# Optimization experiments

Hardware: AMD Instinct MI355X
Metric: run time of the kernel (lower is better)

The kernel has to match this reference:

```python
import jax, jax.numpy as jnp
import numpy as np

NEG = -9.0e9  # the -9000000000.0 sentinel used by the torch code


def _masked_bidir_scores(first, second, fmask, smask):
    """Vectorized form of the BxB python double loop in score_grounding.
    first: (B,N,D), second: (B,L,D), fmask: (B,N), smask: (B,L).
    Returns sent_scores (B,B) and mention_scores (B,N,L) (= diagonal att)."""
    mask = fmask[:, None, :, None] * smask[None, :, None, :]          # (B,B,N,L)
    avg = jnp.where(mask != 0, mask, NEG)
    am_first = jax.nn.softmax(avg, axis=2)                            # softmax over N (dim=0 per pair)
    am_second = jax.nn.softmax(avg, axis=3)                           # softmax over L (dim=1 per pair)
    dot = jnp.einsum('ind,jld->ijnl', first, second)                  # (B,B,N,L)
    attm = dot * mask
    att = jnp.where(attm * mask != 0, attm, NEG)
    aw_first = jax.nn.softmax(att, axis=3) * mask                     # softmax(att, dim=-1)*mask
    aw_second = jnp.transpose(
        jax.nn.softmax(jnp.swapaxes(att, 2, 3), axis=3) * jnp.swapaxes(mask, 2, 3), (0, 1, 3, 2)
    )                                                                 # softmax(att.T,-1)*mask.T, transposed back
    sent = (jnp.sum(aw_first * att * am_first, axis=(2, 3))
            + jnp.sum(aw_second * att * am_second, axis=(2, 3)))      # (B,B)
    B = first.shape[0]
    mention = att[jnp.arange(B), jnp.arange(B)]                       # diagonal pairs (B,N,L)
    return sent, mention


def _pairwise_mlp(first, second, W1, b1, W2, b2, W3, b3):
    # SimplePairWiseClassifier: MLP over cat(first, second, first*second); dropout=0 (eval-deterministic)
    x = jnp.concatenate([first, second, first * second], axis=-1)     # (..., 3D)
    h = jax.nn.relu(x @ W1 + b1)
    h = jax.nn.relu(h @ W2 + b2)
    return (h @ W3 + b3)[..., 0]


def setup_inputs() -> dict:
    key = jax.random.key(0)
    ks = jax.random.split(key, 12)
    B, Nt, Ns, L, D, H = 32, 64, 48, 36, 1024, 1024

    def mask(k, n):
        m = (jax.random.uniform(k, (B, n)) < 0.85).astype(jnp.float32)
        return m.at[:, :2].set(1.0)  # guarantee no all-zero rows

    return {
        'text_embeddings': jax.random.normal(ks[0], (B, Nt, D), jnp.float32),
        'span_embeddings': jax.random.normal(ks[1], (B, Ns, D), jnp.float32),
        'image_embeddings': jax.random.normal(ks[2], (B, L, D), jnp.float32),
        'text_mask': mask(ks[3], Nt),
        'span_mask': mask(ks[4], Ns),
        'image_mask': mask(ks[5], L),
        'W1': jax.random.normal(ks[6], (3 * D, H), jnp.float32) * 0.02,
        'b1': jnp.zeros((H,), jnp.float32),
        'W2': jax.random.normal(ks[7], (H, H), jnp.float32) * 0.02,
        'b2': jnp.zeros((H,), jnp.float32),
        'W3': jax.random.normal(ks[8], (H, 1), jnp.float32) * 0.02,
        'b3': jnp.zeros((1,), jnp.float32),
    }


def reference(text_embeddings, span_embeddings, image_embeddings,
              text_mask, span_mask, image_mask, W1, b1, W2, b2, W3, b3):
    B, Ns, D = span_embeddings.shape
    # calculate_loss
    S, _ = _masked_bidir_scores(text_embeddings, image_embeddings, text_mask, image_mask)
    # span_emb.view(B, N, -1, D).mean(dim=2) is identity for (B,Ns,D)
    _, grounding_scores = _masked_bidir_scores(span_embeddings, image_embeddings, span_mask, image_mask)
    # score_text over all span pairs (itertools.combinations order == triu_indices k=1)
    fi, si = np.triu_indices(Ns, k=1)
    text_scores = _pairwise_mlp(span_embeddings[:, fi], span_embeddings[:, si],
                                W1, b1, W2, b2, W3, b3)               # (B, Ns*(Ns-1)/2)
    # contrastive retrieval loss over the BxB sentence-image score matrix
    loss = -(jnp.trace(jax.nn.log_softmax(S, axis=1))
             + jnp.trace(jax.nn.log_softmax(S.T, axis=1))) / B
    return loss, grounding_scores, text_scores
```

## Files before the change

kernel.cpp:

```cpp
#include <hip/hip_runtime.h>
#include <math.h>
#include <stdint.h>

#define B_    32
#define NT    64
#define NS    48
#define LI    36
#define D_    1024
#define H_    1024
#define NPAIR 1128
#define ROWS  (B_*NPAIR)
#define NEGV  -9.0e9f
#define NROWT 282
#define CPX   36

typedef _Float16 half8 __attribute__((ext_vector_type(8)));
typedef float floatx4 __attribute__((ext_vector_type(4)));
typedef __attribute__((address_space(3))) uint32_t lds_u32;
typedef __attribute__((address_space(1))) const uint32_t glb_u32;

#define GLOAD16(src, dst) __builtin_amdgcn_global_load_lds((glb_u32*)(src), (lds_u32*)(dst), 16, 0, 0)

#define MMQ(QR, QC)                                                            \
  {                                                                            \
    _Pragma("unroll") for (int i = 0; i < 4; ++i) {                            \
      _Pragma("unroll") for (int j = 0; j < 2; ++j) {                          \
        acc[QR * 4 + i][QC * 2 + j] = __builtin_amdgcn_mfma_f32_16x16x32_f16(  \
            aF[i][0], bF[j][0], acc[QR * 4 + i][QC * 2 + j], 0, 0, 0);         \
        acc[QR * 4 + i][QC * 2 + j] = __builtin_amdgcn_mfma_f32_16x16x32_f16(  \
            aF[i][1], bF[j][1], acc[QR * 4 + i][QC * 2 + j], 0, 0, 0);         \
      }                                                                        \
    }                                                                          \
  }

__global__ __launch_bounds__(512, 2) void gemm2_8ph(
    const _Float16* __restrict__ Am, const _Float16* __restrict__ Bt,
    float* __restrict__ scores, const float* __restrict__ bias,
    const float* __restrict__ W3) {
  __shared__ __align__(16) _Float16 sP[65536];
  __shared__ float sRed[256][4];

  const int orig = blockIdx.x;
  const int xcd = orig & 7, pos = orig >> 3;
  const int wg = (xcd < 4 ? xcd * 71 : 284 + (xcd - 4) * 70) + pos;
  const int rowBase = (wg >> 2) * 256;
  const int colBase = (wg & 3) * 256;

  const int t = threadIdx.x;
  const int wave = t >> 6, lane = t & 63;
  const int wq_r = wave >> 2, wq_c = wave & 3;
  const int l15 = lane & 15, l16 = lane >> 4;
  const int sxor = l15 & 7;

  const int srow0 = t >> 3, srow1 = (512 + t) >> 3;
  const int lcol0 = ((t & 7) ^ (srow0 & 7)) << 3;
  const int lcol1 = (((512 + t) & 7) ^ (srow1 & 7)) << 3;
  const _Float16* aS0 = Am + (size_t)(rowBase + srow0) * D_ + lcol0;
  const _Float16* aS1 = Am + (size_t)(rowBase + srow1) * D_ + lcol1;
  const _Float16* bS0 = Bt + (size_t)(colBase + srow0) * D_ + lcol0;
  const _Float16* bS1 = Bt + (size_t)(colBase + srow1) * D_ + lcol1;

  auto stgA = [&](int kt, int h) {
    const int db = kt & 1;
    const size_t so = (size_t)kt * 64 + (size_t)h * 128 * D_;
    _Float16* d = sP + ((db << 1) + h) * 8192;
    GLOAD16(aS0 + so, d + t * 8);
    GLOAD16(aS1 + so, d + 4096 + t * 8);
  };
  auto stgB = [&](int kt, int h) {
    const int db = kt & 1;
    const size_t so = (size_t)kt * 64 + (size_t)h * 128 * D_;
    _Float16* d = sP + 32768 + ((db << 1) + h) * 8192;
    GLOAD16(bS0 + so, d + t * 8);
    GLOAD16(bS1 + so, d + 4096 + t * 8);
  };

  const int aRdRow = (wq_r * 64 + l15) * 64;
  const int bRdRow = (wq_c * 32 + l15) * 64;
  const int rdSlot0 = ((l16) ^ sxor) << 3;
  const int rdSlot1 = ((4 + l16) ^ sxor) << 3;

  half8 aF[4][2], bF[2][2];
  floatx4 acc[8][4] = {};

  auto ldA = [&](int db, int qr) {
    const _Float16* p = sP + ((db << 1) + qr) * 8192 + aRdRow;
#pragma unroll
    for (int i = 0; i < 4; ++i) {
      aF[i][0] = *(const half8*)(p + i * 1024 + rdSlot0);
      aF[i][1] = *(const half8*)(p + i * 1024 + rdSlot1);
    }
  };
  auto ldB = [&](int db, int qc) {
    const _Float16* p = sP + 32768 + ((db << 1) + qc) * 8192 + bRdRow;
#pragma unroll
    for (int j = 0; j < 2; ++j) {
      bF[j][0] = *(const half8*)(p + j * 1024 + rdSlot0);
      bF[j][1] = *(const half8*)(p + j * 1024 + rdSlot1);
    }
  };

  stgB(0, 0); stgA(0, 1); stgA(0, 0); stgB(0, 1); stgB(1, 0); stgA(1, 1);
  asm volatile("s_waitcnt vmcnt(4)" ::: "memory");
  __builtin_amdgcn_s_barrier();

#pragma unroll 1
  for (int kt = 0; kt < 16; ++kt) {
    const int db = kt & 1;
    const int kn1 = (kt + 1) & 15, kn2 = (kt + 2) & 15;
    ldA(db, 0); ldB(db, 0);
    stgA(kn1, 0);
    __builtin_amdgcn_sched_barrier(0);
    __builtin_amdgcn_s_barrier();
    __builtin_amdgcn_s_setprio(1);
    MMQ(0, 0);
    __builtin_amdgcn_s_setprio(0);
    __builtin_amdgcn_s_barrier();
    ldA(db, 1);
    stgB(kn1, 1);
    __builtin_amdgcn_sched_barrier(0);
    __builtin_amdgcn_s_barrier();
    __builtin_amdgcn_s_setprio(1);
    MMQ(1, 0);
    __builtin_amdgcn_s_setprio(0);
    __builtin_amdgcn_s_barrier();
    ldB(db, 1);
    stgB(kn2, 0);
    __builtin_amdgcn_sched_barrier(0);
    __builtin_amdgcn_s_barrier();
    __builtin_amdgcn_s_setprio(1);
    MMQ(1, 1);
    __builtin_amdgcn_s_setprio(0);
    __builtin_amdgcn_s_barrier();
    ldA(db, 0);
    stgA(kn2, 1);
    __builtin_amdgcn_sched_barrier(0);
    asm volatile("s_waitcnt vmcnt(4)" ::: "memory");
    __builtin_amdgcn_s_barrier();
    __builtin_amdgcn_s_setprio(1);
    MMQ(0, 1);
    __builtin_amdgcn_s_setprio(0);
    __builtin_amdgcn_s_barrier();
  }

  float bv[2][2], wv[2][2];
#pragma unroll
  for (int qc = 0; qc < 2; ++qc)
#pragma unroll
    for (int j = 0; j < 2; ++j) {
      int c = colBase + qc * 128 + wq_c * 32 + j * 16 + l15;
      bv[qc][j] = bias[c];
      wv[qc][j] = W3[c];
    }
#pragma unroll
  for (int qr = 0; qr < 2; ++qr)
#pragma unroll
    for (int i = 0; i < 4; ++i)
#pragma unroll
      for (int q = 0; q < 4; ++q) {
        float s = 0.f;
#pragma unroll
        for (int qc = 0; qc < 2; ++qc)
#pragma unroll
          for (int j = 0; j < 2; ++j)
            s += fmaxf(acc[qr * 4 + i][qc * 2 + j][q] + bv[qc][j], 0.f) * wv[qc][j];
        s += __shfl_xor(s, 1); s += __shfl_xor(s, 2);
        s += __shfl_xor(s, 4); s += __shfl_xor(s, 8);
        if (l15 == 0)
          sRed[qr * 128 + wq_r * 64 + i * 16 + l16 * 4 + q][wq_c] = s;
      }
  __syncthreads();
  if (t < 256)
    atomicAdd(&scores[rowBase + t],
              sRed[t][0] + sRed[t][1] + sRed[t][2] + sRed[t][3]);
}

__device__ __forceinline__ void gemm_body(
    const _Float16* __restrict__ A, const _Float16* __restrict__ Bt,
    float* __restrict__ Cf, int N, int K, int rowBase, int colBase) {
  __shared__ __align__(16) _Float16 sA[8192];
  __shared__ __align__(16) _Float16 sB[8192];
  const int tid = threadIdx.x;
  const int lane = tid & 63;
  const int wave = tid >> 6;
  const int wr = wave >> 1, wc = wave & 1;
  const int l15 = lane & 15, l16 = lane >> 4;
  const int rsw = (l15 >> 1) & 3;
  const int sRow = tid >> 2;
  const int swz8 = (((tid & 3) ^ ((tid >> 3) & 3)) << 3);
  const _Float16* gA = A + (size_t)(rowBase + sRow) * K + swz8;
  const _Float16* gB = Bt + (size_t)(colBase + sRow) * K + swz8;
  _Float16* lA = sA + tid * 8;
  _Float16* lB = sB + tid * 8;

  floatx4 acc[4][4] = {};
  for (int k0 = 0; k0 < K; k0 += 64) {
    GLOAD16(gA + k0,               lA);
    GLOAD16(gA + 64 * K + k0,      lA + 2048);
    GLOAD16(gA + k0 + 32,          lA + 4096);
    GLOAD16(gA + 64 * K + k0 + 32, lA + 6144);
    GLOAD16(gB + k0,               lB);
    GLOAD16(gB + 64 * K + k0,      lB + 2048);
    GLOAD16(gB + k0 + 32,          lB + 4096);
    GLOAD16(gB + 64 * K + k0 + 32, lB + 6144);
    __syncthreads();
#pragma unroll
    for (int h = 0; h < 2; ++h) {
      const int hb = h * 4096;
      half8 aF[4], bF[4];
#pragma unroll
      for (int i = 0; i < 4; ++i)
        aF[i] = *(const half8*)&sA[hb + (wr * 64 + i * 16 + l15) * 32 + ((l16 ^ rsw) << 3)];
#pragma unroll
      for (int j = 0; j < 4; ++j)
        bF[j] = *(const half8*)&sB[hb + (wc * 64 + j * 16 + l15) * 32 + ((l16 ^ rsw) << 3)];
#pragma unroll
      for (int i = 0; i < 4; ++i)
#pragma unroll
        for (int j = 0; j < 4; ++j)
          acc[i][j] = __builtin_amdgcn_mfma_f32_16x16x32_f16(aF[i], bF[j], acc[i][j], 0, 0, 0);
    }
    __syncthreads();
  }
#pragma unroll
  for (int i = 0; i < 4; ++i)
#pragma unroll
    for (int q = 0; q < 4; ++q) {
      int r = rowBase + wr * 64 + i * 16 + l16 * 4 + q;
#pragma unroll
      for (int j = 0; j < 4; ++j) {
        int c = colBase + wc * 64 + j * 16 + l15;
        Cf[(size_t)r * N + c] = acc[i][j][q];
      }
    }
}

__global__ __launch_bounds__(256) void gemm_trio(
    const _Float16* __restrict__ textH, const _Float16* __restrict__ imgH,
    const _Float16* __restrict__ spanH, const _Float16* __restrict__ W1abT,
    float* __restrict__ dotTI, float* __restrict__ dotSI, float* __restrict__ AB1) {
  int bid = blockIdx.x;
  if (bid < 144)      gemm_body(textH, imgH, dotTI, 1152, D_, (bid / 9) * 128, (bid % 9) * 128);
  else if (bid < 252) { int b = bid - 144; gemm_body(spanH, imgH, dotSI, 1152, D_, (b / 9) * 128, (b % 9) * 128); }
  else                { int b = bid - 252; gemm_body(spanH, W1abT, AB1, 2048, D_, (b / 16) * 128, (b % 16) * 128); }
}

__global__ __launch_bounds__(256) void gemm1_fused(
    const _Float16* __restrict__ spanH, const _Float16* __restrict__ W1cT,
    const float* __restrict__ AB1, const float* __restrict__ b1,
    _Float16* __restrict__ h1out,
    const int* __restrict__ idxF, const int* __restrict__ idxS) {
  __shared__ __align__(16) _Float16 sF[8192];
  __shared__ __align__(16) _Float16 sS[8192];
  __shared__ __align__(16) _Float16 sB[8192];
  __shared__ int sIF[128], sIS[128];
  int bid = blockIdx.x;
  int x = bid & 7, ord = bid >> 3;
  int rowT = x * CPX + (ord >> 3);
  int colT = ord & 7;
  if (rowT >= NROWT) return;
  const int rowBase = rowT * 128, colBase = colT * 128;
  const int tid = threadIdx.x;
  const int lane = tid & 63;
  const int wave = tid >> 6;
  const int wr = wave >> 1, wc = wave & 1;
  const int l15 = lane & 15, l16 = lane >> 4;
  const int rsw = (l15 >> 1) & 3;

  if (tid < 128) {
    int rg = rowBase + tid;
    sIF[tid] = idxF[rg];
    sIS[tid] = idxS[rg];
  }
  __syncthreads();

  const int sRow = tid >> 2;
  const int swz8 = (((tid & 3) ^ ((tid >> 3) & 3)) << 3);
  const _Float16* gF0 = spanH + (size_t)sIF[sRow] * D_ + swz8;
  const _Float16* gF1 = spanH + (size_t)sIF[sRow + 64] * D_ + swz8;
  const _Float16* gS0 = spanH + (size_t)sIS[sRow] * D_ + swz8;
  const _Float16* gS1 = spanH + (size_t)sIS[sRow + 64] * D_ + swz8;
  const _Float16* gB  = W1cT + (size_t)(colBase + sRow) * D_ + swz8;
  _Float16* lF = sF + tid * 8;
  _Float16* lS = sS + tid * 8;
  _Float16* lB = sB + tid * 8;

  floatx4 acc[4][4] = {};
  for (int k0 = 0; k0 < D_; k0 += 64) {
    GLOAD16(gF0 + k0,      lF);
    GLOAD16(gF1 + k0,      lF + 2048);
    GLOAD16(gF0 + k0 + 32, lF + 4096);
    GLOAD16(gF1 + k0 + 32, lF + 6144);
    GLOAD16(gS0 + k0,      lS);
    GLOAD16(gS1 + k0,      lS + 2048);
    GLOAD16(gS0 + k0 + 32, lS + 4096);
    GLOAD16(gS1 + k0 + 32, lS + 6144);
    GLOAD16(gB + k0,               lB);
    GLOAD16(gB + 64 * D_ + k0,     lB + 2048);
    GLOAD16(gB + k0 + 32,          lB + 4096);
    GLOAD16(gB + 64 * D_ + k0 + 32,lB + 6144);
    __syncthreads();
#pragma unroll
    for (int h = 0; h < 2; ++h) {
      const int hb = h * 4096;
      half8 aF[4], bF[4];
#pragma unroll
      for (int i = 0; i < 4; ++i) {
        int off = hb + (wr * 64 + i * 16 + l15) * 32 + ((l16 ^ rsw) << 3);
        half8 f = *(const half8*)&sF[off];
        half8 s = *(const half8*)&sS[off];
        aF[i] = f * s;
      }
#pragma unroll
      for (int j = 0; j < 4; ++j)
        bF[j] = *(const half8*)&sB[hb + (wc * 64 + j * 16 + l15) * 32 + ((l16 ^ rsw) << 3)];
#pragma unroll
      for (int i = 0; i < 4; ++i)
#pragma unroll
        for (int j = 0; j < 4; ++j)
          acc[i][j] = __builtin_amdgcn_mfma_f32_16x16x32_f16(aF[i], bF[j], acc[i][j], 0, 0, 0);
    }
    __syncthreads();
  }

  int cols[4]; float bv[4];
#pragma unroll
  for (int j = 0; j < 4; ++j) {
    cols[j] = colBase + wc * 64 + j * 16 + l15;
    bv[j] = b1[cols[j]];
  }
#pragma unroll
  for (int i = 0; i < 4; ++i)
#pragma unroll
    for (int q = 0; q < 4; ++q) {
      int rL = wr * 64 + i * 16 + l16 * 4 + q;
      int rG = rowBase + rL;
      const float* ap = AB1 + (size_t)sIF[rL] * 2048;
      const float* bp = AB1 + (size_t)sIS[rL] * 2048 + 1024;
#pragma unroll
      for (int j = 0; j < 4; ++j) {
        int c = cols[j];
        float v = acc[i][j][q] + ap[c] + bp[c] + bv[j];
        h1out[(size_t)rG * 1024 + c] = (_Float16)fmaxf(v, 0.f);
      }
    }
}

__global__ __launch_bounds__(256) void cvt_all(
    const float* __restrict__ text, const float* __restrict__ span,
    const float* __restrict__ img, _Float16* __restrict__ textH,
    _Float16* __restrict__ spanH, _Float16* __restrict__ imgH) {
  long long i = (long long)blockIdx.x * 256 + threadIdx.x;
  const float* src; _Float16* dst; long long off;
  if (i < 262144)      { src = text; dst = textH; off = i; }
  else if (i < 458752) { src = span; dst = spanH; off = i - 262144; }
  else if (i < 606208) { src = img;  dst = imgH;  off = i - 458752; }
  else return;
  const float4* p = (const float4*)src + off * 2;
  float4 a = p[0], b = p[1];
  half8 h;
  h[0] = (_Float16)a.x; h[1] = (_Float16)a.y; h[2] = (_Float16)a.z; h[3] = (_Float16)a.w;
  h[4] = (_Float16)b.x; h[5] = (_Float16)b.y; h[6] = (_Float16)b.z; h[7] = (_Float16)b.w;
  *(half8*)(dst + off * 8) = h;
}

__global__ __launch_bounds__(256) void transpose_all(
    const float* __restrict__ W1, const float* __restrict__ W2,
    _Float16* __restrict__ W1abT, _Float16* __restrict__ W1cT,
    _Float16* __restrict__ W2T) {
  __shared__ float tbuf[32][33];
  const float* in; _Float16* out;
  switch (blockIdx.z) {
    case 0: in = W1;                 out = W1abT;                 break;
    case 1: in = W1 + 1024 * 1024;   out = W1abT + 1024 * 1024;   break;
    case 2: in = W1 + 2048 * 1024;   out = W1cT;                  break;
    default: in = W2;                out = W2T;                   break;
  }
  const int tx = threadIdx.x & 31, ty = threadIdx.x >> 5;
  const int k0 = blockIdx.y * 32, n0 = blockIdx.x * 32;
#pragma unroll
  for (int q = 0; q < 4; ++q)
    tbuf[ty + q * 8][tx] = in[(size_t)(k0 + ty + q * 8) * 1024 + n0 + tx];
  __syncthreads();
#pragma unroll
  for (int q = 0; q < 4; ++q)
    out[(size_t)(n0 + ty + q * 8) * 1024 + k0 + tx] = (_Float16)tbuf[tx][ty + q * 8];
}

__global__ __launch_bounds__(256) void idx_init(int* __restrict__ idxF, int* __restrict__ idxS) {
  int r = blockIdx.x * 256 + threadIdx.x;
  if (r >= ROWS) return;
  int bb = r / NPAIR, p = r - bb * NPAIR;
  int cum = 0, f = 0;
  while (true) { int cnt = NS - 1 - f; if (p < cum + cnt) break; cum += cnt; ++f; }
  idxF[r] = bb * NS + f;
  idxS[r] = bb * NS + f + 1 + (p - cum);
}

__global__ void init_scores(float* __restrict__ scores, const float* __restrict__ b3) {
  int idx = blockIdx.x * 256 + threadIdx.x;
  if (idx < ROWS) scores[idx] = b3[0];
}

__global__ __launch_bounds__(256) void extract_grounding(
    const float* __restrict__ dotSI, const float* __restrict__ smask,
    const float* __restrict__ imask, float* __restrict__ outg) {
  int idx = blockIdx.x * 256 + threadIdx.x;
  if (idx >= B_ * NS * LI) return;
  int b = idx / (NS * LI);
  int rem = idx - b * (NS * LI);
  int n = rem / LI, l = rem - n * LI;
  float v = dotSI[(size_t)(b * NS + n) * (B_ * LI) + b * LI + l];
  outg[idx] = (smask[b * NS + n] * imask[b * LI + l] != 0.f) ? v : NEGV;
}

__global__ __launch_bounds__(64) void sent_kernel(
    const float* __restrict__ dotTI, const float* __restrict__ tmask,
    const float* __restrict__ imask, float* __restrict__ S) {
  const int i = blockIdx.y, j = blockIdx.x, t = threadIdx.x;
  __shared__ float red1[64], red2[64];
  const int stride = B_ * LI;
  float e1 = 0.f;
  {
    float tm = tmask[i * NT + t];
    if (tm != 0.f) {
      const float* row = dotTI + (size_t)(i * NT + t) * stride + j * LI;
      float m = -INFINITY;
      for (int l = 0; l < LI; ++l) if (imask[j * LI + l] != 0.f) m = fmaxf(m, row[l]);
      float z = 0.f, w = 0.f;
      for (int l = 0; l < LI; ++l) if (imask[j * LI + l] != 0.f) {
        float d = row[l], p = expf(d - m);
        z += p; w += p * d;
      }
      e1 = w / z;
    }
  }
  red1[t] = e1;
  float e2 = 0.f;
  if (t < LI) {
    float im = imask[j * LI + t];
    if (im != 0.f) {
      const float* col = dotTI + (size_t)(i * NT) * stride + j * LI + t;
      float m = -INFINITY;
      for (int n = 0; n < NT; ++n) if (tmask[i * NT + n] != 0.f) m = fmaxf(m, col[(size_t)n * stride]);
      float z = 0.f, w = 0.f;
      for (int n = 0; n < NT; ++n) if (tmask[i * NT + n] != 0.f) {
        float d = col[(size_t)n * stride], p = expf(d - m);
        z += p; w += p * d;
      }
      e2 = w / z;
    }
  }
  red2[t] = e2;
  __syncthreads();
  if (t == 0) {
    float s1 = 0.f, s2 = 0.f, cn = 0.f, cl = 0.f;
    for (int n = 0; n < NT; ++n) { s1 += red1[n]; cn += tmask[i * NT + n]; }
    for (int l = 0; l < LI; ++l) { s2 += red2[l]; cl += imask[j * LI + l]; }
    S[i * B_ + j] = s1 / cn + s2 / cl;
  }
}

__global__ __launch_bounds__(64) void loss_kernel(
    const float* __restrict__ S, float* __restrict__ out) {
  __shared__ float sS[B_][B_ + 1];
  __shared__ float acc[B_];
  const int t = threadIdx.x;
  for (int e = t; e < B_ * B_; e += 64) sS[e / B_][e % B_] = S[e];
  __syncthreads();
  if (t < B_) {
    float m = -INFINITY;
    for (int j = 0; j < B_; ++j) m = fmaxf(m, sS[t][j]);
    float z = 0.f;
    for (int j = 0; j < B_; ++j) z += expf(sS[t][j] - m);
    float lr = m + logf(z);
    float m2 = -INFINITY;
    for (int i = 0; i < B_; ++i) m2 = fmaxf(m2, sS[i][t]);
    float z2 = 0.f;
    for (int i = 0; i < B_; ++i) z2 += expf(sS[i][t] - m2);
    float lc = m2 + logf(z2);
    acc[t] = 2.f * sS[t][t] - lr - lc;
  }
  __syncthreads();
  if (t == 0) {
    float s = 0.f;
    for (int i = 0; i < B_; ++i) s += acc[i];
    out[0] = -s / (float)B_;
  }
}

extern "C" void kernel_launch(void* const* d_in, const int* in_sizes, int n_in,
                              void* d_out, int out_size, void* d_ws, size_t ws_size,
                              hipStream_t stream) {
  const float* text  = (const float*)d_in[0];
  const float* span  = (const float*)d_in[1];
  const float* img   = (const float*)d_in[2];
  const float* tmask = (const float*)d_in[3];
  const float* smask = (const float*)d_in[4];
  const float* imask = (const float*)d_in[5];
  const float* W1    = (const float*)d_in[6];
  const float* b1    = (const float*)d_in[7];
  const float* W2    = (const float*)d_in[8];
  const float* b2    = (const float*)d_in[9];
  const float* W3    = (const float*)d_in[10];
  const float* b3    = (const float*)d_in[11];

  float* out     = (float*)d_out;
  float* outLoss = out;
  float* outG    = out + 1;
  float* outT    = out + 1 + (size_t)B_ * NS * LI;

  char* w = (char*)d_ws;
  float*    dotTI = (float*)w;            w += (size_t)(B_*NT) * (B_*LI) * 4;
  float*    dotSI = (float*)w;            w += (size_t)(B_*NS) * (B_*LI) * 4;
  float*    S     = (float*)w;            w += 1024 * 4;
  float*    AB1   = (float*)w;            w += (size_t)1536 * 2048 * 4;
  _Float16* h1    = (_Float16*)w;         w += (size_t)ROWS * 1024 * 2;
  _Float16* textH = (_Float16*)w;         w += (size_t)2048 * 1024 * 2;
  _Float16* spanH = (_Float16*)w;         w += (size_t)1536 * 1024 * 2;
  _Float16* imgH  = (_Float16*)w;         w += (size_t)1152 * 1024 * 2;
  _Float16* W1abT = (_Float16*)w;         w += (size_t)2048 * 1024 * 2;
  _Float16* W1cT  = (_Float16*)w;         w += (size_t)1024 * 1024 * 2;
  _Float16* W2T   = (_Float16*)w;         w += (size_t)1024 * 1024 * 2;
  int*      idxF  = (int*)w;              w += ROWS * 4;
  int*      idxS  = (int*)w;              w += ROWS * 4;
  (void)ws_size; (void)in_sizes; (void)n_in; (void)out_size;

  cvt_all<<<(606208 + 255) / 256, 256, 0, stream>>>(text, span, img, textH, spanH, imgH);
  transpose_all<<<dim3(32, 32, 4), 256, 0, stream>>>(W1, W2, W1abT, W1cT, W2T);
  idx_init<<<(ROWS + 255) / 256, 256, 0, stream>>>(idxF, idxS);

  gemm_trio<<<444, 256, 0, stream>>>(textH, imgH, spanH, W1abT, dotTI, dotSI, AB1);
  sent_kernel<<<dim3(B_, B_), 64, 0, stream>>>(dotTI, tmask, imask, S);
  loss_kernel<<<1, 64, 0, stream>>>(S, outLoss);
  extract_grounding<<<(B_*NS*LI + 255) / 256, 256, 0, stream>>>(dotSI, smask, imask, outG);

  gemm1_fused<<<8 * CPX * 8, 256, 0, stream>>>(spanH, W1cT, AB1, b1, h1, idxF, idxS);
  init_scores<<<(ROWS + 255) / 256, 256, 0, stream>>>(outT, b3);
  gemm2_8ph<<<564, 512, 0, stream>>>(h1, W2T, outT, b2, W3);
}
```

Baseline: 331.1 us.

## Replace gather GEMM1 with 256x256 8-phase pipelined kernel using register-staged products

The old 128x128 gemm1_fused kernel is replaced by gemm1_8ph, a 512-thread 256x256-tile kernel. It uses the same phased MFMA schedule with setprio and XCD-aware block remapping as gemm2. Gathered span rows are loaded into registers, multiplied elementwise, and written once to LDS as the A operand, while the weight tiles go through direct global-to-LDS loads. This removes the per-MFMA re-multiplication of F and S from LDS and halves the operand traffic per output, at the cost of more registers and tighter manual waitcnt sequencing. gemm2's prefetch index masking is also moved inside the staging helpers.

```diff
diff --git a/kernel.cpp b/kernel.cpp
--- a/kernel.cpp
+++ b/kernel.cpp
@@ -11,8 +11,6 @@
 #define NPAIR 1128
 #define ROWS  (B_*NPAIR)
 #define NEGV  -9.0e9f
-#define NROWT 282
-#define CPX   36
 
 typedef _Float16 half8 __attribute__((ext_vector_type(8)));
 typedef float floatx4 __attribute__((ext_vector_type(4)));
@@ -33,6 +31,167 @@
     }                                                                          \
   }
 
+__global__ __launch_bounds__(512, 2) void gemm1_8ph(
+    const _Float16* __restrict__ spanH, const _Float16* __restrict__ W1cT,
+    const float* __restrict__ AB1, const float* __restrict__ b1,
+    _Float16* __restrict__ h1out,
+    const int* __restrict__ idxF, const int* __restrict__ idxS) {
+  __shared__ __align__(16) _Float16 sP[32768];
+  __shared__ int sIF[256], sIS[256];
+
+  const int orig = blockIdx.x;
+  const int xcd = orig & 7, pos = orig >> 3;
+  const int wg = (xcd < 4 ? xcd * 71 : 284 + (xcd - 4) * 70) + pos;
+  const int rowBase = (wg >> 2) * 256;
+  const int colBase = (wg & 3) * 256;
+
+  const int t = threadIdx.x;
+  const int wave = t >> 6, lane = t & 63;
+  const int wq_r = wave >> 2, wq_c = wave & 3;
+  const int l15 = lane & 15, l16 = lane >> 4;
+
+  if (t < 256) { sIF[t] = idxF[rowBase + t]; sIS[t] = idxS[rowBase + t]; }
+  __syncthreads();
+
+  const int srow = t >> 3;
+  const int slot = t & 7;
+  const int wsw = ((slot ^ (srow & 7)) << 3);
+
+  const int oF0a = sIF[srow] << 10,        oF0b = sIF[64 + srow] << 10;
+  const int oS0a = sIS[srow] << 10,        oS0b = sIS[64 + srow] << 10;
+  const int oF1a = sIF[128 + srow] << 10,  oF1b = sIF[192 + srow] << 10;
+  const int oS1a = sIS[128 + srow] << 10,  oS1b = sIS[192 + srow] << 10;
+  const int lcol = slot << 3;
+
+  const _Float16* gB0a = W1cT + (size_t)(colBase + srow) * D_ + wsw;
+  const _Float16* gB0b = W1cT + (size_t)(colBase + 64 + srow) * D_ + wsw;
+  const _Float16* gB1a = W1cT + (size_t)(colBase + 128 + srow) * D_ + wsw;
+  const _Float16* gB1b = W1cT + (size_t)(colBase + 192 + srow) * D_ + wsw;
+
+  half8 rF0a, rF0b, rS0a, rS0b, rF1a, rF1b, rS1a, rS1b;
+
+  #define ISSUE_FS0(kt) {                                            \
+    const int kc = (((kt) & 15) << 6) + lcol;                        \
+    rF0a = *(const half8*)(spanH + oF0a + kc);                       \
+    rF0b = *(const half8*)(spanH + oF0b + kc);                       \
+    rS0a = *(const half8*)(spanH + oS0a + kc);                       \
+    rS0b = *(const half8*)(spanH + oS0b + kc); }
+  #define ISSUE_FS1(kt) {                                            \
+    const int kc = (((kt) & 15) << 6) + lcol;                        \
+    rF1a = *(const half8*)(spanH + oF1a + kc);                       \
+    rF1b = *(const half8*)(spanH + oF1b + kc);                       \
+    rS1a = *(const half8*)(spanH + oS1a + kc);                       \
+    rS1b = *(const half8*)(spanH + oS1b + kc); }
+  #define WRITE_A0() {                                               \
+    *(half8*)(sP + srow * 64 + wsw)        = rF0a * rS0a;            \
+    *(half8*)(sP + 4096 + srow * 64 + wsw) = rF0b * rS0b; }
+  #define WRITE_A1() {                                               \
+    *(half8*)(sP + 8192 + srow * 64 + wsw)  = rF1a * rS1a;           \
+    *(half8*)(sP + 12288 + srow * 64 + wsw) = rF1b * rS1b; }
+  #define STG_B0(kt) {                                               \
+    const int kc = (((kt) & 15) << 6);                               \
+    GLOAD16(gB0a + kc, sP + 16384 + t * 8);                          \
+    GLOAD16(gB0b + kc, sP + 20480 + t * 8); }
+  #define STG_B1(kt) {                                               \
+    const int kc = (((kt) & 15) << 6);                               \
+    GLOAD16(gB1a + kc, sP + 24576 + t * 8);                          \
+    GLOAD16(gB1b + kc, sP + 28672 + t * 8); }
+
+  const int rsw = l15 & 7;
+  const int aRd = (wq_r * 64 + l15) * 64;
+  const int bRd = (wq_c * 32 + l15) * 64;
+  const int rd0 = ((l16) ^ rsw) << 3;
+  const int rd1 = ((4 + l16) ^ rsw) << 3;
+  half8 aF[4][2], bF[2][2];
+  floatx4 acc[8][4] = {};
+  #define LDA(h) {                                                   \
+    const _Float16* p = sP + (h) * 8192 + aRd;                       \
+    _Pragma("unroll") for (int i = 0; i < 4; ++i) {                  \
+      aF[i][0] = *(const half8*)(p + i * 1024 + rd0);                \
+      aF[i][1] = *(const half8*)(p + i * 1024 + rd1); } }
+  #define LDB(h) {                                                   \
+    const _Float16* p = sP + 16384 + (h) * 8192 + bRd;               \
+    _Pragma("unroll") for (int j = 0; j < 2; ++j) {                  \
+      bF[j][0] = *(const half8*)(p + j * 1024 + rd0);                \
+      bF[j][1] = *(const half8*)(p + j * 1024 + rd1); } }
+
+  ISSUE_FS0(0); ISSUE_FS1(0); STG_B0(0);
+  asm volatile("s_waitcnt vmcnt(6)" ::: "memory");
+  WRITE_A0();
+  asm volatile("s_waitcnt lgkmcnt(0)" ::: "memory");
+  __builtin_amdgcn_sched_barrier(0);
+  __builtin_amdgcn_s_barrier();
+
+#pragma unroll 1
+  for (int kt = 0; kt < 16; ++kt) {
+    STG_B1(kt);
+    ISSUE_FS0(kt + 1);
+    asm volatile("s_waitcnt vmcnt(6)" ::: "memory");
+    WRITE_A1();
+    LDA(0); LDB(0);
+    asm volatile("s_waitcnt lgkmcnt(0)" ::: "memory");
+    __builtin_amdgcn_sched_barrier(0);
+    __builtin_amdgcn_s_barrier();
+    __builtin_amdgcn_s_setprio(1);
+    MMQ(0, 0);
+    __builtin_amdgcn_s_setprio(0);
+    __builtin_amdgcn_s_barrier();
+    ISSUE_FS1(kt + 1);
+    LDA(1);
+    __builtin_amdgcn_sched_barrier(0);
+    __builtin_amdgcn_s_barrier();
+    __builtin_amdgcn_s_setprio(1);
+    MMQ(1, 0);
+    __builtin_amdgcn_s_setprio(0);
+    __builtin_amdgcn_s_barrier();
+    STG_B0(kt + 1);
+    asm volatile("s_waitcnt vmcnt(10)" ::: "memory");
+    LDA(0); LDB(1);
+    __builtin_amdgcn_sched_barrier(0);
+    __builtin_amdgcn_s_barrier();
+    __builtin_amdgcn_s_setprio(1);
+    MMQ(0, 1);
+    __builtin_amdgcn_s_setprio(0);
+    __builtin_amdgcn_s_barrier();
+    asm volatile("s_waitcnt vmcnt(6)" ::: "memory");
+    WRITE_A0();
+    LDA(1);
+    asm volatile("s_waitcnt lgkmcnt(0)" ::: "memory");
+    __builtin_amdgcn_sched_barrier(0);
+    __builtin_amdgcn_s_barrier();
+    __builtin_amdgcn_s_setprio(1);
+    MMQ(1, 1);
+    __builtin_amdgcn_s_setprio(0);
+    __builtin_amdgcn_s_barrier();
+  }
+
+  float bv[2][2];
+#pragma unroll
+  for (int qc = 0; qc < 2; ++qc)
+#pragma unroll
+    for (int j = 0; j < 2; ++j)
+      bv[qc][j] = b1[colBase + qc * 128 + wq_c * 32 + j * 16 + l15];
+#pragma unroll
+  for (int qr = 0; qr < 2; ++qr)
+#pragma unroll
+    for (int i = 0; i < 4; ++i)
+#pragma unroll
+      for (int q = 0; q < 4; ++q) {
+        int rL = qr * 128 + wq_r * 64 + i * 16 + l16 * 4 + q;
+        const float* ap = AB1 + (size_t)sIF[rL] * 2048;
+        const float* bp = AB1 + (size_t)sIS[rL] * 2048 + 1024;
+        size_t ro = (size_t)(rowBase + rL) * 1024;
+#pragma unroll
+        for (int qc = 0; qc < 2; ++qc)
+#pragma unroll
+          for (int j = 0; j < 2; ++j) {
+            int c = colBase + qc * 128 + wq_c * 32 + j * 16 + l15;
+            float v = acc[qr * 4 + i][qc * 2 + j][q] + ap[c] + bp[c] + bv[qc][j];
+            h1out[ro + c] = (_Float16)fmaxf(v, 0.f);
+          }
+      }
+}
+
 __global__ __launch_bounds__(512, 2) void gemm2_8ph(
     const _Float16* __restrict__ Am, const _Float16* __restrict__ Bt,
     float* __restrict__ scores, const float* __restrict__ bias,
@@ -62,14 +221,14 @@
 
   auto stgA = [&](int kt, int h) {
     const int db = kt & 1;
-    const size_t so = (size_t)kt * 64 + (size_t)h * 128 * D_;
+    const size_t so = (size_t)(kt & 15) * 64 + (size_t)h * 128 * D_;
     _Float16* d = sP + ((db << 1) + h) * 8192;
     GLOAD16(aS0 + so, d + t * 8);
     GLOAD16(aS1 + so, d + 4096 + t * 8);
   };
   auto stgB = [&](int kt, int h) {
     const int db = kt & 1;
-    const size_t so = (size_t)kt * 64 + (size_t)h * 128 * D_;
+    const size_t so = (size_t)(kt & 15) * 64 + (size_t)h * 128 * D_;
     _Float16* d = sP + 32768 + ((db << 1) + h) * 8192;
     GLOAD16(bS0 + so, d + t * 8);
     GLOAD16(bS1 + so, d + 4096 + t * 8);
@@ -107,7 +266,7 @@
 #pragma unroll 1
   for (int kt = 0; kt < 16; ++kt) {
     const int db = kt & 1;
-    const int kn1 = (kt + 1) & 15, kn2 = (kt + 2) & 15;
+    const int kn1 = kt + 1, kn2 = kt + 2;
     ldA(db, 0); ldB(db, 0);
     stgA(kn1, 0);
     __builtin_amdgcn_sched_barrier(0);
@@ -243,107 +402,6 @@
   if (bid < 144)      gemm_body(textH, imgH, dotTI, 1152, D_, (bid / 9) * 128, (bid % 9) * 128);
   else if (bid < 252) { int b = bid - 144; gemm_body(spanH, imgH, dotSI, 1152, D_, (b / 9) * 128, (b % 9) * 128); }
   else                { int b = bid - 252; gemm_body(spanH, W1abT, AB1, 2048, D_, (b / 16) * 128, (b % 16) * 128); }
-}
-
-__global__ __launch_bounds__(256) void gemm1_fused(
-    const _Float16* __restrict__ spanH, const _Float16* __restrict__ W1cT,
-    const float* __restrict__ AB1, const float* __restrict__ b1,
-    _Float16* __restrict__ h1out,
-    const int* __restrict__ idxF, const int* __restrict__ idxS) {
-  __shared__ __align__(16) _Float16 sF[8192];
-  __shared__ __align__(16) _Float16 sS[8192];
-  __shared__ __align__(16) _Float16 sB[8192];
-  __shared__ int sIF[128], sIS[128];
-  int bid = blockIdx.x;
-  int x = bid & 7, ord = bid >> 3;
-  int rowT = x * CPX + (ord >> 3);
-  int colT = ord & 7;
-  if (rowT >= NROWT) return;
-  const int rowBase = rowT * 128, colBase = colT * 128;
-  const int tid = threadIdx.x;
-  const int lane = tid & 63;
-  const int wave = tid >> 6;
-  const int wr = wave >> 1, wc = wave & 1;
-  const int l15 = lane & 15, l16 = lane >> 4;
-  const int rsw = (l15 >> 1) & 3;
-
-  if (tid < 128) {
-    int rg = rowBase + tid;
-    sIF[tid] = idxF[rg];
-    sIS[tid] = idxS[rg];
-  }
-  __syncthreads();
-
-  const int sRow = tid >> 2;
-  const int swz8 = (((tid & 3) ^ ((tid >> 3) & 3)) << 3);
-  const _Float16* gF0 = spanH + (size_t)sIF[sRow] * D_ + swz8;
-  const _Float16* gF1 = spanH + (size_t)sIF[sRow + 64] * D_ + swz8;
-  const _Float16* gS0 = spanH + (size_t)sIS[sRow] * D_ + swz8;
-  const _Float16* gS1 = spanH + (size_t)sIS[sRow + 64] * D_ + swz8;
-  const _Float16* gB  = W1cT + (size_t)(colBase + sRow) * D_ + swz8;
-  _Float16* lF = sF + tid * 8;
-  _Float16* lS = sS + tid * 8;
-  _Float16* lB = sB + tid * 8;
-
-  floatx4 acc[4][4] = {};
-  for (int k0 = 0; k0 < D_; k0 += 64) {
-    GLOAD16(gF0 + k0,      lF);
-    GLOAD16(gF1 + k0,      lF + 2048);
-    GLOAD16(gF0 + k0 + 32, lF + 4096);
-    GLOAD16(gF1 + k0 + 32, lF + 6144);
-    GLOAD16(gS0 + k0,      lS);
-    GLOAD16(gS1 + k0,      lS + 2048);
-    GLOAD16(gS0 + k0 + 32, lS + 4096);
-    GLOAD16(gS1 + k0 + 32, lS + 6144);
-    GLOAD16(gB + k0,               lB);
-    GLOAD16(gB + 64 * D_ + k0,     lB + 2048);
-    GLOAD16(gB + k0 + 32,          lB + 4096);
-    GLOAD16(gB + 64 * D_ + k0 + 32,lB + 6144);
-    __syncthreads();
-#pragma unroll
-    for (int h = 0; h < 2; ++h) {
-      const int hb = h * 4096;
-      half8 aF[4], bF[4];
-#pragma unroll
-      for (int i = 0; i < 4; ++i) {
-        int off = hb + (wr * 64 + i * 16 + l15) * 32 + ((l16 ^ rsw) << 3);
-        half8 f = *(const half8*)&sF[off];
-        half8 s = *(const half8*)&sS[off];
-        aF[i] = f * s;
-      }
-#pragma unroll
-      for (int j = 0; j < 4; ++j)
-        bF[j] = *(const half8*)&sB[hb + (wc * 64 + j * 16 + l15) * 32 + ((l16 ^ rsw) << 3)];
-#pragma unroll
-      for (int i = 0; i < 4; ++i)
-#pragma unroll
-        for (int j = 0; j < 4; ++j)
-          acc[i][j] = __builtin_amdgcn_mfma_f32_16x16x32_f16(aF[i], bF[j], acc[i][j], 0, 0, 0);
-    }
-    __syncthreads();
-  }
-
-  int cols[4]; float bv[4];
-#pragma unroll
-  for (int j = 0; j < 4; ++j) {
-    cols[j] = colBase + wc * 64 + j * 16 + l15;
-    bv[j] = b1[cols[j]];
-  }
-#pragma unroll
-  for (int i = 0; i < 4; ++i)
-#pragma unroll
-    for (int q = 0; q < 4; ++q) {
-      int rL = wr * 64 + i * 16 + l16 * 4 + q;
-      int rG = rowBase + rL;
-      const float* ap = AB1 + (size_t)sIF[rL] * 2048;
-      const float* bp = AB1 + (size_t)sIS[rL] * 2048 + 1024;
-#pragma unroll
-      for (int j = 0; j < 4; ++j) {
-        int c = cols[j];
-        float v = acc[i][j][q] + ap[c] + bp[c] + bv[j];
-        h1out[(size_t)rG * 1024 + c] = (_Float16)fmaxf(v, 0.f);
-      }
-    }
 }
 
 __global__ __launch_bounds__(256) void cvt_all(
@@ -535,7 +593,7 @@
   loss_kernel<<<1, 64, 0, stream>>>(S, outLoss);
   extract_grounding<<<(B_*NS*LI + 255) / 256, 256, 0, stream>>>(dotSI, smask, imask, outG);
 
-  gemm1_fused<<<8 * CPX * 8, 256, 0, stream>>>(spanH, W1cT, AB1, b1, h1, idxF, idxS);
+  gemm1_8ph<<<564, 512, 0, stream>>>(spanH, W1cT, AB1, b1, h1, idxF, idxS);
   init_scores<<<(ROWS + 255) / 256, 256, 0, stream>>>(outT, b3);
   gemm2_8ph<<<564, 512, 0, stream>>>(h1, W2T, outT, b2, W3);
 }
```

After: 350.0 us. 1.06x slower.
